# Performance work log

Hardware: AMD Instinct MI355X
Metric: run time of the kernel (lower is better)

The kernel has to match this reference:

```python
import jax, jax.numpy as jnp
import numpy as np

CLASSES = 100
SIGMA = 1.0
K_MIX = 11   # mixup pseudo-label kNN
K_KNN = 3    # knn regularizer


def _pairwise_sq(a, b):
    # ||a_i - b_j||^2 via Gram trick; a:[M,D], b:[N,D] -> [M,N]
    aa = jnp.sum(a * a, axis=1)[:, None]
    bb = jnp.sum(b * b, axis=1)[None, :]
    return aa + bb - 2.0 * (a @ b.T)


def _mode_rows(vals):
    # vals: [M,K] float labels. torch.mode semantics: most frequent value,
    # smallest value on ties.
    eq = vals[:, :, None] == vals[:, None, :]      # [M,K,K]
    counts = jnp.sum(eq.astype(vals.dtype), axis=2)  # [M,K]
    maxc = jnp.max(counts, axis=1, keepdims=True)
    masked = jnp.where(counts == maxc, vals, jnp.inf)
    return jnp.min(masked, axis=1)


def setup_inputs() -> dict:
    key = jax.random.key(0)
    k1, k2, k3, k4 = jax.random.split(key, 4)
    N, D = 4096, 512
    x = jax.random.normal(k1, (N, D), dtype=jnp.float32)
    y = jax.random.randint(k2, (N,), 0, CLASSES).astype(jnp.float32)
    lam = jax.random.beta(k3, 2.0, 2.0, (), dtype=jnp.float32)  # Beta(alpha=2, alpha=2)
    perm = jax.random.permutation(k4, N).astype(jnp.int32)
    return {"x": x, "y": y, "lam": lam, "perm": perm}


def reference(x, y, lam, perm):
    # ---- mixup branch: pseudo-label mixed samples via k=11 NN mode ----
    x_ul = x * lam + x[perm] * (1.0 - lam)              # [N,D]
    d = _pairwise_sq(x_ul, x)                            # [N,N]
    _, idx = jax.lax.top_k(-d, K_MIX)                    # indices of k smallest dists
    y_ul = _mode_rows(y[idx])                            # [N]
    x = jnp.concatenate([x, x_ul], axis=0)               # [2N,D]
    y = jnp.concatenate([y, y_ul], axis=0)               # [2N]

    num = x.shape[0]
    y_int = y.astype(jnp.int32)
    # per-class means (empty classes masked out, as the torch loop skips them)
    counts = jax.ops.segment_sum(jnp.ones((num,), x.dtype), y_int, num_segments=CLASSES)
    mu = jax.ops.segment_sum(x, y_int, num_segments=CLASSES) / jnp.maximum(counts, 1.0)[:, None]
    d2 = _pairwise_sq(x, mu)                             # [num, classes]
    pi = jnp.exp(-d2 / (2.0 * SIGMA ** 2)) * (counts > 0).astype(x.dtype)[None, :]
    yh = jax.nn.one_hot(y_int, CLASSES, dtype=x.dtype)
    eps = 1e-15
    pi = pi / (jnp.sum(pi, axis=1, keepdims=True) + eps)
    pi = jnp.clip(pi, 0.0, 1.0)
    loss_gm = jnp.mean(jnp.sum((pi - yh) ** 2, axis=1))

    # ---- knn regularizer: k=3 NN (excluding self) mode label, MSE ----
    dk = _pairwise_sq(x, x)                              # [num,num]
    _, idxk = jax.lax.top_k(-dk, K_KNN + 1)              # nearest is self (dist 0)
    y_ng = _mode_rows(y[idxk[:, 1:]])
    loss_knn = jnp.mean((y_ng - y) ** 2)
    return loss_gm + 0.01 * loss_knn
```

## Files before the change

### kernel.cpp

```cpp
#include <hip/hip_runtime.h>
#include <math.h>

#define N0   4096
#define D    512
#define NUM  8192
#define NCLS 100
#define KMIX 11

#define OFF_NALL   0
#define OFF_YALL   8192
#define OFF_RLOSS  16384
#define OFF_KSQ    24576
#define OFF_MUSUM  32768
#define OFF_CNT    83968
#define OFF_KNN    84096
#define ZERO_N     51344
#define OFF_NMU    84112
#define OFF_MUT    84224
#define OFF_TK1S   135424
#define OFF_TK1I   659712
#define OFF_TK2S   1184000
#define OFF_TK2I   1446144
#define OFF_XH     1708288
#define TOTAL_F    3805440
#define NEED_BYTES ((size_t)TOTAL_F * 4)

typedef _Float16 half8 __attribute__((ext_vector_type(8)));
typedef _Float16 half4v __attribute__((ext_vector_type(4)));
typedef float f32x4 __attribute__((ext_vector_type(4)));
typedef unsigned long long u64;

__device__ __forceinline__ float4 ld_row4(const float* __restrict__ x, const int* __restrict__ perm,
                                          float lam, float om, int r, int col) {
  if (r < N0) {
    return *(const float4*)(x + (size_t)r * D + col);
  } else {
    int rr = r - N0;
    int p = perm[rr];
    float4 a = *(const float4*)(x + (size_t)rr * D + col);
    float4 b = *(const float4*)(x + (size_t)p * D + col);
    float4 m;
    m.x = lam * a.x + om * b.x;  m.y = lam * a.y + om * b.y;
    m.z = lam * a.z + om * b.z;  m.w = lam * a.w + om * b.w;
    return m;
  }
}

__device__ __forceinline__ void gld_lds16(const _Float16* g, _Float16* l) {
  __builtin_amdgcn_global_load_lds(
      (const __attribute__((address_space(1))) void*)g,
      (__attribute__((address_space(3))) void*)l, 16, 0, 0);
}

__device__ __forceinline__ unsigned sortable(float s) {
  unsigned u = __float_as_uint(s);
  return ((int)u < 0) ? ~u : (u | 0x80000000u);
}
__device__ __forceinline__ float unsortable(unsigned u) {
  return __uint_as_float(((int)u < 0) ? (u & 0x7fffffffu) : ~u);
}

__global__ __launch_bounds__(256) void k_zero(float* __restrict__ p, int n) {
  int i = blockIdx.x * 256 + threadIdx.x;
  if (i < n) p[i] = 0.f;
}

__global__ __launch_bounds__(256) void k_y(const float* __restrict__ y, float* __restrict__ y_all) {
  int i = blockIdx.x * 256 + threadIdx.x;
  if (i < N0) y_all[i] = y[i];
}

__global__ __launch_bounds__(64) void k_prep(const float* __restrict__ x, const float* __restrict__ y,
                                             const int* __restrict__ perm, const float* __restrict__ lam_p,
                                             _Float16* __restrict__ Xh, float* __restrict__ n_all,
                                             float* __restrict__ y_all, float* __restrict__ accp,
                                             int* __restrict__ donep) {
  int i = blockIdx.x;
  float lam = lam_p[0], om = 1.0f - lam;
  int t = threadIdx.x;
  float4 a = ld_row4(x, perm, lam, om, i, t * 4);
  float4 b = ld_row4(x, perm, lam, om, i, t * 4 + 256);
  half4v ha, hb;
  ha.x = (_Float16)a.x; ha.y = (_Float16)a.y; ha.z = (_Float16)a.z; ha.w = (_Float16)a.w;
  hb.x = (_Float16)b.x; hb.y = (_Float16)b.y; hb.z = (_Float16)b.z; hb.w = (_Float16)b.w;
  *(half4v*)(Xh + (size_t)i * D + t * 4) = ha;
  *(half4v*)(Xh + (size_t)i * D + t * 4 + 256) = hb;
  float s = a.x*a.x + a.y*a.y + a.z*a.z + a.w*a.w
          + b.x*b.x + b.y*b.y + b.z*b.z + b.w*b.w;
  #pragma unroll
  for (int o = 32; o > 0; o >>= 1) s += __shfl_down(s, o, 64);
  if (t == 0) {
    n_all[i] = s;
    if (i < N0) y_all[i] = y[i];
    if (i == 0) { accp[0] = 0.f; donep[0] = 0; }
  }
}

template<int M, int NSPL>
__device__ __forceinline__ void knn_body(const _Float16* __restrict__ Xq,
                                         const _Float16* __restrict__ Xc,
                                         const float* __restrict__ nC,
                                         int cb0, int nctiles, int row0, int split,
                                         float* __restrict__ outS, int* __restrict__ outI,
                                         char* smem) {
  _Float16* Sh = (_Float16*)smem;
  u64* Lb = (u64*)smem;

  int tid = threadIdx.x;
  int wave = tid >> 6, lane = tid & 63;
  int wq = wave >> 1, wc = wave & 1;
  int col16 = lane & 15, quad = lane >> 4;

  const _Float16* q0 = Xq + (size_t)(wq * 32 + col16) * D + quad * 8;
  const _Float16* q1 = q0 + (size_t)16 * D;
  half8 aR[8][2][2];
  #pragma unroll
  for (int kt = 0; kt < 8; kt++)
    #pragma unroll
    for (int h = 0; h < 2; h++) {
      aR[kt][0][h] = *(const half8*)(q0 + kt * 64 + h * 32);
      aR[kt][1][h] = *(const half8*)(q1 + kt * 64 + h * 32);
    }

  u64 keys[M];
  #pragma unroll
  for (int q = 0; q < M; q++) keys[q] = ~0ULL;

  int r_scan = tid & 63, h_scan = tid >> 6;

  for (int ct = 0; ct < nctiles; ct++) {
    int c0 = cb0 + ct * 128;
    const _Float16* bb = Xc + (size_t)(c0 + wc * 64 + col16) * D + quad * 8;

    f32x4 acc[2][4];
    #pragma unroll
    for (int i = 0; i < 2; i++)
      #pragma unroll
      for (int j = 0; j < 4; j++) acc[i][j] = (f32x4){0.f, 0.f, 0.f, 0.f};

    #pragma unroll
    for (int kt = 0; kt < 8; kt++) {
      half8 b[4][2];
      #pragma unroll
      for (int j = 0; j < 4; j++)
        #pragma unroll
        for (int h = 0; h < 2; h++)
          b[j][h] = *(const half8*)(bb + (size_t)(j * 16) * D + kt * 64 + h * 32);
      #pragma unroll
      for (int h = 0; h < 2; h++)
        #pragma unroll
        for (int i = 0; i < 2; i++)
          #pragma unroll
          for (int j = 0; j < 4; j++)
            acc[i][j] = __builtin_amdgcn_mfma_f32_16x16x32_f16(aR[kt][i][h], b[j][h], acc[i][j], 0, 0, 0);
    }

    #pragma unroll
    for (int j = 0; j < 4; j++) {
      int cl = wc * 64 + j * 16 + col16;
      float ncv = nC[c0 + cl];
      #pragma unroll
      for (int i = 0; i < 2; i++) {
        half4v st;
        st.x = (_Float16)(ncv - 2.f * acc[i][j][0]);
        st.y = (_Float16)(ncv - 2.f * acc[i][j][1]);
        st.z = (_Float16)(ncv - 2.f * acc[i][j][2]);
        st.w = (_Float16)(ncv - 2.f * acc[i][j][3]);
        *(half4v*)&Sh[(size_t)cl * 68 + wq * 32 + i * 16 + quad * 4] = st;
      }
    }
    __syncthreads();

    for (int c = h_scan * 32; c < h_scan * 32 + 32; c++) {
      float s = (float)Sh[c * 68 + r_scan];
      u64 key = ((u64)sortable(s) << 32) | (unsigned)(c0 + c);
      if (key < keys[M - 1]) {
        keys[M - 1] = key;
        #pragma unroll
        for (int p = M - 1; p > 0; p--) {
          if (keys[p] < keys[p - 1]) { u64 tmp = keys[p]; keys[p] = keys[p - 1]; keys[p - 1] = tmp; }
        }
      }
    }
    __syncthreads();
  }

  #pragma unroll
  for (int q = 0; q < M; q++)
    Lb[((size_t)h_scan * 64 + r_scan) * M + q] = keys[q];
  __syncthreads();
  if (tid < 64) {
    int p0 = 0, p1 = 0, p2 = 0, p3 = 0;
    const u64* L0 = Lb + (size_t)(0 * 64 + tid) * M;
    const u64* L1 = Lb + (size_t)(1 * 64 + tid) * M;
    const u64* L2 = Lb + (size_t)(2 * 64 + tid) * M;
    const u64* L3 = Lb + (size_t)(3 * 64 + tid) * M;
    size_t off = (size_t)(row0 + tid) * ((size_t)NSPL * M) + (size_t)split * M;
    #pragma unroll
    for (int q = 0; q < M; q++) {
      u64 k0 = (p0 < M) ? L0[p0] : ~0ULL;
      u64 k1 = (p1 < M) ? L1[p1] : ~0ULL;
      u64 k2 = (p2 < M) ? L2[p2] : ~0ULL;
      u64 k3 = (p3 < M) ? L3[p3] : ~0ULL;
      u64 b01 = k0 < k1 ? k0 : k1;
      u64 b23 = k2 < k3 ? k2 : k3;
      u64 b = b01 < b23 ? b01 : b23;
      if (b == k0) p0++; else if (b == k1) p1++; else if (b == k2) p2++; else p3++;
      outS[off + q] = unsortable((unsigned)(b >> 32));
      outI[off + q] = (int)(unsigned)b;
    }
  }
}

__global__ __launch_bounds__(256, 2) void k_knn_all(const _Float16* __restrict__ Xh,
                                                    const float* __restrict__ n_all,
                                                    float* __restrict__ tk1s, int* __restrict__ tk1i,
                                                    float* __restrict__ tk2s, int* __restrict__ tk2i) {
  __shared__ __align__(16) char smem[32768];
  int bx = blockIdx.x;
  if (bx < 512) {
    int qblk = bx & 127, split = bx >> 7;
    knn_body<8, 4>(Xh + (size_t)(qblk * 64) * D, Xh, n_all,
                   split * 2048, 16, qblk * 64, split, tk2s, tk2i, smem);
  } else {
    int b = bx - 512;
    int qblk = b & 63, split = b >> 6;
    knn_body<16, 8>(Xh + (size_t)(N0 + qblk * 64) * D, Xh, n_all,
                    split * 512, 4, qblk * 64, split, tk1s, tk1i, smem);
  }
}

__global__ __launch_bounds__(256) void k_rr1(const float* __restrict__ x, const int* __restrict__ perm,
                                             const float* __restrict__ lam_p,
                                             const float* __restrict__ tks, const int* __restrict__ tki,
                                             const float* __restrict__ n_all, const float* __restrict__ y,
                                             float* __restrict__ y_all) {
  __shared__ u64 kl[128];
  __shared__ int sidx[16];
  __shared__ float sdot[16];
  int i = blockIdx.x;
  int t = threadIdx.x;
  float lam = lam_p[0], om = 1.f - lam;
  if (t < 128) {
    float s = tks[(size_t)i * 128 + t];
    int id = tki[(size_t)i * 128 + t];
    kl[t] = ((u64)sortable(s) << 32) | (unsigned)id;
  }
  __syncthreads();
  if (t < 128) {
    u64 me = kl[t];
    int rank = 0;
    for (int j = 0; j < 128; j++) rank += (kl[j] < me) ? 1 : 0;
    if (rank < 16) sidx[rank] = (int)(unsigned)me;
  }
  __syncthreads();
  int g = t >> 4, l16 = t & 15;
  int c = sidx[g];
  float dot = 0.f;
  for (int d0 = l16 * 4; d0 < D; d0 += 64) {
    float4 q4 = ld_row4(x, perm, lam, om, N0 + i, d0);
    float4 c4 = *(const float4*)(x + (size_t)c * D + d0);
    dot += q4.x*c4.x + q4.y*c4.y + q4.z*c4.z + q4.w*c4.w;
  }
  #pragma unroll
  for (int o = 8; o > 0; o >>= 1) dot += __shfl_down(dot, o, 16);
  if (l16 == 0) sdot[g] = n_all[c] - 2.f * dot;
  __syncthreads();
  if (t == 0) {
    float es[16]; int ei[16];
    for (int q = 0; q < 16; q++) { es[q] = sdot[q]; ei[q] = sidx[q]; }
    for (int a = 1; a < 16; a++) {
      float s = es[a]; int id = ei[a];
      int b = a - 1;
      while (b >= 0 && (es[b] > s || (es[b] == s && ei[b] > id))) {
        es[b + 1] = es[b]; ei[b + 1] = ei[b]; b--;
      }
      es[b + 1] = s; ei[b + 1] = id;
    }
    float lab[KMIX];
    for (int q = 0; q < KMIX; q++) lab[q] = y[ei[q]];
    float best = 3.0e38f; int bestc = 0;
    for (int q = 0; q < KMIX; q++) {
      int cnt = 0;
      for (int r = 0; r < KMIX; r++) cnt += (lab[r] == lab[q]) ? 1 : 0;
      if (cnt > bestc || (cnt == bestc && lab[q] < best)) { bestc = cnt; best = lab[q]; }
    }
    y_all[N0 + i] = best;
  }
}

__global__ __launch_bounds__(256) void k_post2(const float* __restrict__ x, const int* __restrict__ perm,
                                               const float* __restrict__ lam_p,
                                               const float* __restrict__ tks, const int* __restrict__ tki,
                                               const float* __restrict__ n_all, const float* __restrict__ y_all,
                                               float* __restrict__ ksq,
                                               _Float16* __restrict__ muH, float* __restrict__ nmu_pad,
                                               float* __restrict__ counts) {
  __shared__ __align__(16) char sm[33824];
  int bx = blockIdx.x;
  int t = threadIdx.x;
  float lam = lam_p[0], om = 1.f - lam;

  if (bx < NUM) {
    u64* kl = (u64*)sm;
    int* sidx = (int*)(sm + 256);
    float* sdot = (float*)(sm + 288);
    int i = bx;
    if (t < 32) {
      float s = tks[(size_t)i * 32 + t];
      int id = tki[(size_t)i * 32 + t];
      kl[t] = ((u64)sortable(s) << 32) | (unsigned)id;
    }
    __syncthreads();
    if (t < 32) {
      u64 me = kl[t];
      int rank = 0;
      #pragma unroll
      for (int j = 0; j < 32; j++) rank += (kl[j] < me) ? 1 : 0;
      if (rank < 8) sidx[rank] = (int)(unsigned)me;
    }
    __syncthreads();
    int g = t >> 5, l32 = t & 31;
    int c = sidx[g];
    float dot = 0.f;
    for (int d0 = l32 * 4; d0 < D; d0 += 128) {
      float4 q4 = ld_row4(x, perm, lam, om, i, d0);
      float4 c4 = ld_row4(x, perm, lam, om, c, d0);
      dot += q4.x*c4.x + q4.y*c4.y + q4.z*c4.z + q4.w*c4.w;
    }
    #pragma unroll
    for (int o = 16; o > 0; o >>= 1) dot += __shfl_down(dot, o, 32);
    if (l32 == 0) sdot[g] = n_all[c] - 2.f * dot;
    __syncthreads();
    if (t == 0) {
      float es[8]; int ei[8];
      for (int q = 0; q < 8; q++) { es[q] = sdot[q]; ei[q] = sidx[q]; }
      for (int a = 1; a < 8; a++) {
        float s = es[a]; int id = ei[a];
        int b = a - 1;
        while (b >= 0 && (es[b] > s || (es[b] == s && ei[b] > id))) {
          es[b + 1] = es[b]; ei[b + 1] = ei[b]; b--;
        }
        es[b + 1] = s; ei[b + 1] = id;
      }
      float l1 = y_all[ei[1]], l2 = y_all[ei[2]], l3 = y_all[ei[3]];
      int c1 = 1 + (int)(l2 == l1) + (int)(l3 == l1);
      int c2 = 1 + (int)(l1 == l2) + (int)(l3 == l2);
      int c3 = 1 + (int)(l1 == l3) + (int)(l2 == l3);
      int mc = c1 > c2 ? c1 : c2; mc = mc > c3 ? mc : c3;
      float mv = 3.0e38f;
      if (c1 == mc) mv = fminf(mv, l1);
      if (c2 == mc) mv = fminf(mv, l2);
      if (c3 == mc) mv = fminf(mv, l3);
      float d = mv - y_all[i];
      ksq[i] = d * d;
    }
  } else {
    int c = bx - NUM;
    int* lst = (int*)sm;
    float* red = (float*)(sm + 32768);
    int* cntp = (int*)(sm + 33792);
    if (c >= NCLS) {
      for (int d = t; d < D; d += 256) muH[(size_t)c * D + d] = (_Float16)0.f;
      if (t == 0) { nmu_pad[c] = 0.f; counts[c] = 0.f; }
      return;
    }
    float fc = (float)c;
    if (t == 0) cntp[0] = 0;
    __syncthreads();
    for (int i = t; i < NUM; i += 256) {
      if (y_all[i] == fc) {
        int pos = atomicAdd(cntp, 1);
        int p = (i >= N0) ? perm[i - N0] : 0;
        lst[pos] = i | (p << 13);
      }
    }
    __syncthreads();
    int n = cntp[0];
    float a0 = 0.f, a1 = 0.f;
    for (int m = 0; m < n; m++) {
      int v = lst[m];
      int i = v & 8191;
      if (i < N0) {
        a0 += x[(size_t)i * D + t];
        a1 += x[(size_t)i * D + t + 256];
      } else {
        int rr = i - N0, p = v >> 13;
        a0 += lam * x[(size_t)rr * D + t] + om * x[(size_t)p * D + t];
        a1 += lam * x[(size_t)rr * D + t + 256] + om * x[(size_t)p * D + t + 256];
      }
    }
    float inv = 1.f / fmaxf((float)n, 1.f);
    float v0 = a0 * inv, v1 = a1 * inv;
    muH[(size_t)c * D + t] = (_Float16)v0;
    muH[(size_t)c * D + t + 256] = (_Float16)v1;
    red[t] = v0 * v0 + v1 * v1;
    __syncthreads();
    for (int o = 128; o > 0; o >>= 1) { if (t < o) red[t] += red[t + o]; __syncthreads(); }
    if (t == 0) { nmu_pad[c] = red[0]; counts[c] = (float)n; }
  }
}

__global__ __launch_bounds__(256) void k_gm2f(const _Float16* __restrict__ Xh,
                                              const _Float16* __restrict__ muH,
                                              const float* __restrict__ nmu_pad,
                                              const float* __restrict__ counts,
                                              const float* __restrict__ n_all,
                                              const float* __restrict__ y_all,
                                              const float* __restrict__ ksq,
                                              float* __restrict__ accp, int* __restrict__ donep,
                                              float* __restrict__ out) {
  __shared__ __align__(16) char smem[49152];
  float* Ss = (float*)smem;
  _Float16* St = (_Float16*)smem;

  int tid = threadIdx.x;
  int wave = tid >> 6, lane = tid & 63;
  int wq = wave >> 1, wc = wave & 1;
  int col16 = lane & 15, quad = lane >> 4;
  int qb = blockIdx.x * 64;

  const _Float16* qg = Xh + (size_t)(qb + wave * 16 + col16) * D + quad * 8;
  int csegA = 2 * wave, csegB = 2 * wave + 1;
  const _Float16* cgA = muH + (size_t)(csegA * 16 + col16) * D + quad * 8;
  const _Float16* cgB = cgA + (size_t)16 * D;
  int ldsQ = wave * 1024 + lane * 8;
  int ldsCA = 4096 + csegA * 1024 + lane * 8;
  int ldsCB = 4096 + csegB * 1024 + lane * 8;

  f32x4 acc[2][4];
  #pragma unroll
  for (int i = 0; i < 2; i++)
    #pragma unroll
    for (int j = 0; j < 4; j++) acc[i][j] = (f32x4){0.f, 0.f, 0.f, 0.f};

  gld_lds16(qg,       St + ldsQ);
  gld_lds16(qg + 32,  St + ldsQ + 512);
  gld_lds16(cgA,      St + ldsCA);
  gld_lds16(cgA + 32, St + ldsCA + 512);
  gld_lds16(cgB,      St + ldsCB);
  gld_lds16(cgB + 32, St + ldsCB + 512);
  __syncthreads();

  #pragma unroll
  for (int t = 0; t < 8; t++) {
    const int cur = t & 1;
    if (t < 7) {
      int kk = (t + 1) * 64;
      _Float16* B = St + (cur ^ 1) * 12288;
      gld_lds16(qg + kk,       B + ldsQ);
      gld_lds16(qg + kk + 32,  B + ldsQ + 512);
      gld_lds16(cgA + kk,      B + ldsCA);
      gld_lds16(cgA + kk + 32, B + ldsCA + 512);
      gld_lds16(cgB + kk,      B + ldsCB);
      gld_lds16(cgB + kk + 32, B + ldsCB + 512);
    }
    const _Float16* Bc = St + cur * 12288;
    half8 a[2][2], b[4][2];
    #pragma unroll
    for (int i = 0; i < 2; i++)
      #pragma unroll
      for (int h = 0; h < 2; h++)
        a[i][h] = *(const half8*)(Bc + (wq * 2 + i) * 1024 + h * 512 + lane * 8);
    #pragma unroll
    for (int j = 0; j < 4; j++)
      #pragma unroll
      for (int h = 0; h < 2; h++)
        b[j][h] = *(const half8*)(Bc + 4096 + (wc * 4 + j) * 1024 + h * 512 + lane * 8);
    #pragma unroll
    for (int h = 0; h < 2; h++)
      #pragma unroll
      for (int i = 0; i < 2; i++)
        #pragma unroll
        for (int j = 0; j < 4; j++)
          acc[i][j] = __builtin_amdgcn_mfma_f32_16x16x32_f16(a[i][h], b[j][h], acc[i][j], 0, 0, 0);
    __syncthreads();
  }

  #pragma unroll
  for (int j = 0; j < 4; j++) {
    int c_local = wc * 64 + j * 16 + col16;
    float ncv = nmu_pad[c_local];
    #pragma unroll
    for (int i = 0; i < 2; i++) {
      float4 st;
      st.x = ncv - 2.f * acc[i][j][0];
      st.y = ncv - 2.f * acc[i][j][1];
      st.z = ncv - 2.f * acc[i][j][2];
      st.w = ncv - 2.f * acc[i][j][3];
      *(float4*)&Ss[(size_t)c_local * 68 + wq * 32 + i * 16 + quad * 4] = st;
    }
  }
  __syncthreads();

  int r = tid & 63, h = tid >> 6;
  float* redm = (float*)(smem + 35840);
  float* mrow = (float*)(smem + 36864);
  float* Sp   = (float*)(smem + 37120);
  float* Ep   = (float*)(smem + 38144);
  float* Yp   = (float*)(smem + 39168);
  float* Rf   = (float*)(smem + 40192);

  float mymin = 3.0e38f;
  for (int c = h * 32; c < h * 32 + 32; c++) {
    if (c < NCLS && counts[c] > 0.f) mymin = fminf(mymin, Ss[c * 68 + r]);
  }
  redm[h * 64 + r] = mymin;
  __syncthreads();
  if (tid < 64) {
    float ms = fminf(fminf(redm[tid], redm[64 + tid]), fminf(redm[128 + tid], redm[192 + tid]));
    mrow[tid] = ms;
  }
  __syncthreads();
  float ms = mrow[r];
  int yc = (int)y_all[qb + r];
  float Sv = 0.f, Se2 = 0.f, ey = 0.f;
  for (int c = h * 32; c < h * 32 + 32; c++) {
    if (c < NCLS && counts[c] > 0.f) {
      float e = expf(-0.5f * (Ss[c * 68 + r] - ms));
      Sv += e; Se2 += e * e;
      if (c == yc) ey = e;
    }
  }
  Sp[h * 64 + r] = Sv; Ep[h * 64 + r] = Se2; Yp[h * 64 + r] = ey;
  __syncthreads();
  if (tid < 64) {
    float S4 = Sp[tid] + Sp[64 + tid] + Sp[128 + tid] + Sp[192 + tid];
    float E4 = Ep[tid] + Ep[64 + tid] + Ep[128 + tid] + Ep[192 + tid];
    float Y4 = Yp[tid] + Yp[64 + tid] + Yp[128 + tid] + Yp[192 + tid];
    float m = n_all[qb + tid] + mrow[tid];
    float E = expf(-0.5f * m);
    float denom = E * S4 + 1e-15f;
    float f = E / denom;
    float row = E4 * f * f - 2.f * Y4 * f + 1.f + 0.01f * ksq[qb + tid];
    #pragma unroll
    for (int o = 32; o > 0; o >>= 1) row += __shfl_down(row, o, 64);
    Rf[tid] = row;
  }
  __syncthreads();
  if (tid == 0) {
    atomicAdd(accp, Rf[0]);
    __threadfence();
    int old = atomicAdd(donep, 1);
    if (old == (int)gridDim.x - 1) {
      float v = atomicAdd(accp, 0.0f);
      out[0] = v / (float)NUM;
    }
  }
}

#define QT 32
#define CTF 128
#define BKF 32

__global__ __launch_bounds__(64) void k_norms(const float* __restrict__ x, const int* __restrict__ perm,
                                              const float* __restrict__ lam_p, float* __restrict__ n_all) {
  int i = blockIdx.x;
  float lam = lam_p[0], om = 1.0f - lam;
  int t = threadIdx.x;
  float4 a = ld_row4(x, perm, lam, om, i, t * 4);
  float4 b = ld_row4(x, perm, lam, om, i, t * 4 + 256);
  float s = a.x*a.x + a.y*a.y + a.z*a.z + a.w*a.w
          + b.x*b.x + b.y*b.y + b.z*b.z + b.w*b.w;
  #pragma unroll
  for (int o = 32; o > 0; o >>= 1) s += __shfl_down(s, o, 64);
  if (t == 0) n_all[i] = s;
}

template<int KK>
__global__ __launch_bounds__(256) void k_knn_f32(const float* __restrict__ x, const int* __restrict__ perm,
                                                 const float* __restrict__ lam_p, int qstart,
                                                 const float* __restrict__ nC, int candPerSplit, int nsplits,
                                                 float* __restrict__ outS, int* __restrict__ outI) {
  __shared__ float Qs[BKF][QT + 4];
  __shared__ float Cs[BKF][CTF + 4];
  __shared__ float Sf[QT][CTF + 4];

  int tid = threadIdx.x;
  float lam = lam_p[0], om = 1.0f - lam;
  int qbase = blockIdx.x * QT;
  int cb = blockIdx.y * candPerSplit;
  int ce = cb + candPerSplit;

  int cx = tid & 31;
  int ry = tid >> 5;
  int lr = tid >> 3;
  int kc = (tid & 7) * 4;

  float ks[KK]; int ki[KK];
  #pragma unroll
  for (int q = 0; q < KK; q++) { ks[q] = 3.0e38f; ki[q] = 0x7fffffff; }

  for (int c0 = cb; c0 < ce; c0 += CTF) {
    float acc[4][4];
    #pragma unroll
    for (int i = 0; i < 4; i++)
      #pragma unroll
      for (int j = 0; j < 4; j++) acc[i][j] = 0.f;

    for (int kk = 0; kk < D; kk += BKF) {
      __syncthreads();
      {
        float4 v = ld_row4(x, perm, lam, om, qstart + qbase + lr, kk + kc);
        Qs[kc + 0][lr] = v.x; Qs[kc + 1][lr] = v.y; Qs[kc + 2][lr] = v.z; Qs[kc + 3][lr] = v.w;
      }
      #pragma unroll
      for (int rr = 0; rr < 4; rr++) {
        int r = lr + rr * 32;
        float4 v = ld_row4(x, perm, lam, om, c0 + r, kk + kc);
        Cs[kc + 0][r] = v.x; Cs[kc + 1][r] = v.y; Cs[kc + 2][r] = v.z; Cs[kc + 3][r] = v.w;
      }
      __syncthreads();
      #pragma unroll
      for (int k = 0; k < BKF; k++) {
        float4 a4 = *(const float4*)&Qs[k][ry * 4];
        float4 b4 = *(const float4*)&Cs[k][cx * 4];
        float av[4] = {a4.x, a4.y, a4.z, a4.w};
        float bv[4] = {b4.x, b4.y, b4.z, b4.w};
        #pragma unroll
        for (int i = 0; i < 4; i++)
          #pragma unroll
          for (int j = 0; j < 4; j++) acc[i][j] += av[i] * bv[j];
      }
    }
    __syncthreads();
    {
      float4 nc4 = *(const float4*)&nC[c0 + cx * 4];
      float ncv[4] = {nc4.x, nc4.y, nc4.z, nc4.w};
      #pragma unroll
      for (int i = 0; i < 4; i++)
        #pragma unroll
        for (int j = 0; j < 4; j++)
          Sf[ry * 4 + i][cx * 4 + j] = ncv[j] - 2.0f * acc[i][j];
    }
    __syncthreads();
    if (tid < QT) {
      for (int c = 0; c < CTF; c++) {
        float s = Sf[tid][c];
        int j = c0 + c;
        bool worse = (s > ks[KK - 1]) || (s == ks[KK - 1] && j > ki[KK - 1]);
        if (!worse) {
          ks[KK - 1] = s; ki[KK - 1] = j;
          #pragma unroll
          for (int p = KK - 1; p > 0; p--) {
            bool sw = (ks[p] < ks[p - 1]) || (ks[p] == ks[p - 1] && ki[p] < ki[p - 1]);
            if (sw) {
              float ts = ks[p]; ks[p] = ks[p - 1]; ks[p - 1] = ts;
              int ti = ki[p]; ki[p] = ki[p - 1]; ki[p - 1] = ti;
            }
          }
        }
      }
    }
  }

  if (tid < QT) {
    int row = qbase + tid;
    size_t off = (size_t)row * (nsplits * KK) + (size_t)blockIdx.y * KK;
    #pragma unroll
    for (int q = 0; q < KK; q++) { outS[off + q] = ks[q]; outI[off + q] = ki[q]; }
  }
}

__global__ __launch_bounds__(256) void k_final1(const float* __restrict__ tks, const int* __restrict__ tki,
                                                const float* __restrict__ y, float* __restrict__ y_all) {
  int i = blockIdx.x * 256 + threadIdx.x;
  if (i >= N0) return;
  const float* sb = tks + (size_t)i * 44;
  const int* ib = tki + (size_t)i * 44;
  int p0 = 0, p1 = 0, p2 = 0, p3 = 0;
  float lab[KMIX];
  #pragma unroll
  for (int q = 0; q < KMIX; q++) {
    float bs = 3.0e38f; int bi = 0x7fffffff; int w = 0;
    if (p0 < 11) { float s = sb[p0];      int id = ib[p0];      if (s < bs || (s == bs && id < bi)) { bs = s; bi = id; w = 0; } }
    if (p1 < 11) { float s = sb[11 + p1]; int id = ib[11 + p1]; if (s < bs || (s == bs && id < bi)) { bs = s; bi = id; w = 1; } }
    if (p2 < 11) { float s = sb[22 + p2]; int id = ib[22 + p2]; if (s < bs || (s == bs && id < bi)) { bs = s; bi = id; w = 2; } }
    if (p3 < 11) { float s = sb[33 + p3]; int id = ib[33 + p3]; if (s < bs || (s == bs && id < bi)) { bs = s; bi = id; w = 3; } }
    if (w == 0) p0++; else if (w == 1) p1++; else if (w == 2) p2++; else p3++;
    lab[q] = y[bi];
  }
  float best = 3.0e38f; int bestc = 0;
  #pragma unroll
  for (int q = 0; q < KMIX; q++) {
    int c = 0;
    #pragma unroll
    for (int r = 0; r < KMIX; r++) c += (lab[r] == lab[q]) ? 1 : 0;
    if (c > bestc || (c == bestc && lab[q] < best)) { bestc = c; best = lab[q]; }
  }
  y_all[N0 + i] = best;
}

__global__ __launch_bounds__(128) void k_stats(const float* __restrict__ x, const int* __restrict__ perm,
                                               const float* __restrict__ lam_p, const float* __restrict__ y_all,
                                               float* __restrict__ mu_sum, float* __restrict__ counts) {
  int i = blockIdx.x;
  float lam = lam_p[0], om = 1.0f - lam;
  int c = (int)y_all[i];
  float* ms = mu_sum + (size_t)c * D;
  int t = threadIdx.x;
  float4 v = ld_row4(x, perm, lam, om, i, t * 4);
  atomicAdd(&ms[t * 4 + 0], v.x);
  atomicAdd(&ms[t * 4 + 1], v.y);
  atomicAdd(&ms[t * 4 + 2], v.z);
  atomicAdd(&ms[t * 4 + 3], v.w);
  if (t == 0) atomicAdd(&counts[c], 1.0f);
}

__global__ __launch_bounds__(256) void k_mufin(const float* __restrict__ mu_sum, const float* __restrict__ counts,
                                               float* __restrict__ muT, float* __restrict__ nmu) {
  __shared__ float red[256];
  int c = blockIdx.x;
  float inv = 1.0f / fmaxf(counts[c], 1.0f);
  int t = threadIdx.x;
  float v0 = mu_sum[(size_t)c * D + t] * inv;
  float v1 = mu_sum[(size_t)c * D + t + 256] * inv;
  muT[(size_t)t * NCLS + c] = v0;
  muT[(size_t)(t + 256) * NCLS + c] = v1;
  red[t] = v0 * v0 + v1 * v1;
  __syncthreads();
  for (int o = 128; o > 0; o >>= 1) { if (t < o) red[t] += red[t + o]; __syncthreads(); }
  if (t == 0) nmu[c] = red[0];
}

__global__ __launch_bounds__(256) void k_final2(const float* __restrict__ t2s, const int* __restrict__ t2i,
                                                const float* __restrict__ y_all, float* __restrict__ knn_acc) {
  __shared__ float red[256];
  int i = blockIdx.x * 256 + threadIdx.x;
  float dd2 = 0.f;
  if (i < NUM) {
    const float* sA = t2s + (size_t)i * 8; const float* sB = sA + 4;
    const int* iA = t2i + (size_t)i * 8;   const int* iB = iA + 4;
    int pa = 0, pb = 0;
    int midx[4];
    #pragma unroll
    for (int q = 0; q < 4; q++) {
      float sa = (pa < 4) ? sA[pa] : 3.0e38f;
      float sb = (pb < 4) ? sB[pb] : 3.0e38f;
      int ia = (pa < 4) ? iA[pa] : 0x7fffffff;
      int ib = (pb < 4) ? iB[pb] : 0x7fffffff;
      bool ta = (sa < sb) || (sa == sb && ia < ib);
      midx[q] = ta ? ia : ib;
      if (ta) pa++; else pb++;
    }
    float l1 = y_all[midx[1]], l2 = y_all[midx[2]], l3 = y_all[midx[3]];
    int c1 = 1 + (int)(l2 == l1) + (int)(l3 == l1);
    int c2 = 1 + (int)(l1 == l2) + (int)(l3 == l2);
    int c3 = 1 + (int)(l1 == l3) + (int)(l2 == l3);
    int mc = c1 > c2 ? c1 : c2; mc = mc > c3 ? mc : c3;
    float mv = 3.0e38f;
    if (c1 == mc) mv = fminf(mv, l1);
    if (c2 == mc) mv = fminf(mv, l2);
    if (c3 == mc) mv = fminf(mv, l3);
    float d = mv - y_all[i];
    dd2 = d * d;
  }
  red[threadIdx.x] = dd2;
  __syncthreads();
  for (int o = 128; o > 0; o >>= 1) { if (threadIdx.x < o) red[threadIdx.x] += red[threadIdx.x + o]; __syncthreads(); }
  if (threadIdx.x == 0) atomicAdd(knn_acc, red[0]);
}

__global__ __launch_bounds__(128) void k_gm(const float* __restrict__ x, const int* __restrict__ perm,
                                            const float* __restrict__ lam_p, const float* __restrict__ y_all,
                                            const float* __restrict__ n_all, const float* __restrict__ muT,
                                            const float* __restrict__ nmu, const float* __restrict__ counts,
                                            float* __restrict__ row_loss) {
  __shared__ float red[128];
  int i = blockIdx.x;
  int t = threadIdx.x;
  float lam = lam_p[0], om = 1.0f - lam;
  bool valid = (t < NCLS) && (counts[t] > 0.f);
  float d2 = 3.0e38f;
  if (t < NCLS) {
    float dot = 0.f;
    for (int d = 0; d < D; d += 4) {
      float4 v = ld_row4(x, perm, lam, om, i, d);
      dot += v.x * muT[(size_t)(d + 0) * NCLS + t];
      dot += v.y * muT[(size_t)(d + 1) * NCLS + t];
      dot += v.z * muT[(size_t)(d + 2) * NCLS + t];
      dot += v.w * muT[(size_t)(d + 3) * NCLS + t];
    }
    d2 = n_all[i] + nmu[t] - 2.f * dot;
  }
  red[t] = valid ? d2 : 3.0e38f;
  __syncthreads();
  for (int o = 64; o > 0; o >>= 1) { if (t < o) red[t] = fminf(red[t], red[t + o]); __syncthreads(); }
  float m = red[0];
  __syncthreads();
  float e = valid ? expf(-0.5f * (d2 - m)) : 0.f;
  red[t] = e;
  __syncthreads();
  for (int o = 64; o > 0; o >>= 1) { if (t < o) red[t] += red[t + o]; __syncthreads(); }
  float S = red[0];
  __syncthreads();
  float E = expf(-0.5f * m);
  float denom = E * S + 1e-15f;
  float pi = e * E / denom;
  pi = fminf(fmaxf(pi, 0.f), 1.f);
  int yc = (int)y_all[i];
  float term = pi * pi - 2.f * ((t == yc) ? pi : 0.f);
  red[t] = valid ? term : 0.f;
  __syncthreads();
  for (int o = 64; o > 0; o >>= 1) { if (t < o) red[t] += red[t + o]; __syncthreads(); }
  if (t == 0) row_loss[i] = red[0] + 1.0f;
}

__global__ __launch_bounds__(256) void k_final_slow(const float* __restrict__ row_loss,
                                                    const float* __restrict__ knn_acc, float* __restrict__ out) {
  __shared__ float red[256];
  int t = threadIdx.x;
  float s = 0.f;
  for (int i = t; i < NUM; i += 256) s += row_loss[i];
  red[t] = s;
  __syncthreads();
  for (int o = 128; o > 0; o >>= 1) { if (t < o) red[t] += red[t + o]; __syncthreads(); }
  if (t == 0) out[0] = red[0] / (float)NUM + 0.01f * (knn_acc[0] / (float)NUM);
}

extern "C" void kernel_launch(void* const* d_in, const int* in_sizes, int n_in,
                              void* d_out, int out_size, void* d_ws, size_t ws_size,
                              hipStream_t stream) {
  const float* x   = (const float*)d_in[0];
  const float* y   = (const float*)d_in[1];
  const float* lam = (const float*)d_in[2];
  const int* perm  = (const int*)d_in[3];
  float* ws = (float*)d_ws;

  float* n_all  = ws + OFF_NALL;
  float* y_all  = ws + OFF_YALL;
  float* rloss  = ws + OFF_RLOSS;
  float* ksq    = ws + OFF_KSQ;
  float* mu_sum = ws + OFF_MUSUM;
  float* counts = ws + OFF_CNT;
  float* knn_acc= ws + OFF_KNN;
  float* nmu    = ws + OFF_NMU;
  float* muT    = ws + OFF_MUT;
  float* tk1s   = ws + OFF_TK1S;
  int*   tk1i   = (int*)(ws + OFF_TK1I);
  float* tk2s   = ws + OFF_TK2S;
  int*   tk2i   = (int*)(ws + OFF_TK2I);
  _Float16* Xh  = (_Float16*)(ws + OFF_XH);
  _Float16* muH = (_Float16*)(ws + OFF_MUSUM);
  float* nmu_pad= ws + OFF_MUT;
  float* accp   = ws + OFF_KNN;
  int*   donep  = (int*)(ws + OFF_KNN + 1);

  bool fast = ws_size >= NEED_BYTES;

  if (fast) {
    k_prep<<<NUM, 64, 0, stream>>>(x, y, perm, lam, Xh, n_all, y_all, accp, donep);
    k_knn_all<<<1024, 256, 0, stream>>>(Xh, n_all, tk1s, tk1i, tk2s, tk2i);
    k_rr1<<<N0, 256, 0, stream>>>(x, perm, lam, tk1s, tk1i, n_all, y, y_all);
    k_post2<<<NUM + 128, 256, 0, stream>>>(x, perm, lam, tk2s, tk2i, n_all, y_all,
                                           ksq, muH, nmu_pad, counts);
    k_gm2f<<<NUM / 64, 256, 0, stream>>>(Xh, muH, nmu_pad, counts, n_all, y_all,
                                         ksq, accp, donep, (float*)d_out);
  } else {
    k_y<<<(N0 + 255) / 256, 256, 0, stream>>>(y, y_all);
    k_zero<<<(ZERO_N + 255) / 256, 256, 0, stream>>>(mu_sum, ZERO_N);
    k_norms<<<NUM, 64, 0, stream>>>(x, perm, lam, n_all);
    dim3 g1(N0 / QT, 4);
    k_knn_f32<KMIX><<<g1, 256, 0, stream>>>(x, perm, lam, N0, n_all, N0 / 4, 4, tk1s, tk1i);
    k_final1<<<(N0 + 255) / 256, 256, 0, stream>>>(tk1s, tk1i, y, y_all);
    k_stats<<<NUM, 128, 0, stream>>>(x, perm, lam, y_all, mu_sum, counts);
    k_mufin<<<NCLS, 256, 0, stream>>>(mu_sum, counts, muT, nmu);
    dim3 g2(NUM / QT, 2);
    k_knn_f32<4><<<g2, 256, 0, stream>>>(x, perm, lam, 0, n_all, NUM / 2, 2, tk2s, tk2i);
    k_final2<<<NUM / 256, 256, 0, stream>>>(tk2s, tk2i, y_all, knn_acc);
    k_gm<<<NUM, 128, 0, stream>>>(x, perm, lam, y_all, n_all, muT, nmu, counts, rloss);
    k_final_slow<<<1, 256, 0, stream>>>(rloss, knn_acc, (float*)d_out);
  }
}
```

Measured before the change: 783.3 us.

## Fuse mixup and self kNN candidate scans with LDS double-buffered MFMA tiles

The two separate kNN passes over the 8192-row concatenated set are merged. Mixed-sample query rows now compute one distance tile against 1024-column splits of all candidates and feed both the top-8 list (self kNN) and a top-16 list (mixup kNN restricted to splits covering the original rows), so the mixup distances are no longer recomputed. Query and candidate fragments are streamed through double-buffered LDS with direct global-to-LDS loads instead of being held in registers, and occupancy is raised to 3 blocks per CU. This adds extra sort work in the scan loop and a per-k-step barrier, and changes the candidate counts the rerank kernels merge.

Result: faster. 689.2 us (-12.0%).

```diff
diff --git a/kernel.cpp b/kernel.cpp
--- a/kernel.cpp
+++ b/kernel.cpp
@@ -18,9 +18,9 @@
 #define OFF_NMU    84112
 #define OFF_MUT    84224
 #define OFF_TK1S   135424
-#define OFF_TK1I   659712
-#define OFF_TK2S   1184000
-#define OFF_TK2I   1446144
+#define OFF_TK1I   397568
+#define OFF_TK2S   659712
+#define OFF_TK2I   1184000
 #define OFF_XH     1708288
 #define TOTAL_F    3805440
 #define NEED_BYTES ((size_t)TOTAL_F * 4)
@@ -96,14 +96,15 @@
   }
 }
 
-template<int M, int NSPL>
-__device__ __forceinline__ void knn_body(const _Float16* __restrict__ Xq,
-                                         const _Float16* __restrict__ Xc,
-                                         const float* __restrict__ nC,
-                                         int cb0, int nctiles, int row0, int split,
-                                         float* __restrict__ outS, int* __restrict__ outI,
-                                         char* smem) {
-  _Float16* Sh = (_Float16*)smem;
+__device__ __forceinline__ void knn_body_fused(
+    const _Float16* __restrict__ Xq, const _Float16* __restrict__ Xc,
+    const float* __restrict__ nC, int cb0, int nctiles,
+    int row0, int split, bool mix, int mixrow0,
+    float* __restrict__ outS, int* __restrict__ outI,
+    float* __restrict__ outS2, int* __restrict__ outI2,
+    char* smem) {
+  _Float16* St = (_Float16*)smem;
+  _Float16* Sh = (_Float16*)(smem + 24576);
   u64* Lb = (u64*)smem;
 
   int tid = threadIdx.x;
@@ -111,26 +112,34 @@
   int wq = wave >> 1, wc = wave & 1;
   int col16 = lane & 15, quad = lane >> 4;
 
-  const _Float16* q0 = Xq + (size_t)(wq * 32 + col16) * D + quad * 8;
-  const _Float16* q1 = q0 + (size_t)16 * D;
-  half8 aR[8][2][2];
-  #pragma unroll
-  for (int kt = 0; kt < 8; kt++)
-    #pragma unroll
-    for (int h = 0; h < 2; h++) {
-      aR[kt][0][h] = *(const half8*)(q0 + kt * 64 + h * 32);
-      aR[kt][1][h] = *(const half8*)(q1 + kt * 64 + h * 32);
-    }
-
-  u64 keys[M];
-  #pragma unroll
-  for (int q = 0; q < M; q++) keys[q] = ~0ULL;
+  const _Float16* qg = Xq + (size_t)(wave * 16 + col16) * D + quad * 8;
+  int csegA = 2 * wave, csegB = 2 * wave + 1;
+  int ldsQ = wave * 1024 + lane * 8;
+  int ldsCA = 4096 + csegA * 1024 + lane * 8;
+  int ldsCB = 4096 + csegB * 1024 + lane * 8;
+
+  u64 keys[8];
+  #pragma unroll
+  for (int q = 0; q < 8; q++) keys[q] = ~0ULL;
+  u64 keys2[16];
+  #pragma unroll
+  for (int q = 0; q < 16; q++) keys2[q] = ~0ULL;
 
   int r_scan = tid & 63, h_scan = tid >> 6;
+
+  {
+    const _Float16* cA = Xc + (size_t)(cb0 + csegA * 16 + col16) * D + quad * 8;
+    const _Float16* cB = cA + (size_t)16 * D;
+    gld_lds16(qg,      St + ldsQ);  gld_lds16(qg + 32, St + ldsQ + 512);
+    gld_lds16(cA,      St + ldsCA); gld_lds16(cA + 32, St + ldsCA + 512);
+    gld_lds16(cB,      St + ldsCB); gld_lds16(cB + 32, St + ldsCB + 512);
+  }
+  __syncthreads();
 
   for (int ct = 0; ct < nctiles; ct++) {
     int c0 = cb0 + ct * 128;
-    const _Float16* bb = Xc + (size_t)(c0 + wc * 64 + col16) * D + quad * 8;
+    const _Float16* cgA = Xc + (size_t)(c0 + csegA * 16 + col16) * D + quad * 8;
+    const _Float16* cgB = cgA + (size_t)16 * D;
 
     f32x4 acc[2][4];
     #pragma unroll
@@ -139,20 +148,41 @@
       for (int j = 0; j < 4; j++) acc[i][j] = (f32x4){0.f, 0.f, 0.f, 0.f};
 
     #pragma unroll
-    for (int kt = 0; kt < 8; kt++) {
-      half8 b[4][2];
+    for (int t = 0; t < 8; t++) {
+      const int cur = t & 1;
+      if (t < 7) {
+        int kk = (t + 1) * 64;
+        _Float16* B = St + (cur ^ 1) * 12288;
+        gld_lds16(qg + kk,       B + ldsQ);  gld_lds16(qg + kk + 32,  B + ldsQ + 512);
+        gld_lds16(cgA + kk,      B + ldsCA); gld_lds16(cgA + kk + 32, B + ldsCA + 512);
+        gld_lds16(cgB + kk,      B + ldsCB); gld_lds16(cgB + kk + 32, B + ldsCB + 512);
+      } else if (ct + 1 < nctiles) {
+        const _Float16* nA = cgA + (size_t)128 * D;
+        const _Float16* nB = cgB + (size_t)128 * D;
+        gld_lds16(qg,      St + ldsQ);  gld_lds16(qg + 32, St + ldsQ + 512);
+        gld_lds16(nA,      St + ldsCA); gld_lds16(nA + 32, St + ldsCA + 512);
+        gld_lds16(nB,      St + ldsCB); gld_lds16(nB + 32, St + ldsCB + 512);
+      }
+      const _Float16* Bc = St + cur * 12288;
+      half8 a[2][2], b[4][2];
+      #pragma unroll
+      for (int i = 0; i < 2; i++)
+        #pragma unroll
+        for (int h = 0; h < 2; h++)
+          a[i][h] = *(const half8*)(Bc + (wq * 2 + i) * 1024 + h * 512 + lane * 8);
       #pragma unroll
       for (int j = 0; j < 4; j++)
         #pragma unroll
         for (int h = 0; h < 2; h++)
-          b[j][h] = *(const half8*)(bb + (size_t)(j * 16) * D + kt * 64 + h * 32);
+          b[j][h] = *(const half8*)(Bc + 4096 + (wc * 4 + j) * 1024 + h * 512 + lane * 8);
       #pragma unroll
       for (int h = 0; h < 2; h++)
         #pragma unroll
         for (int i = 0; i < 2; i++)
           #pragma unroll
           for (int j = 0; j < 4; j++)
-            acc[i][j] = __builtin_amdgcn_mfma_f32_16x16x32_f16(aR[kt][i][h], b[j][h], acc[i][j], 0, 0, 0);
+            acc[i][j] = __builtin_amdgcn_mfma_f32_16x16x32_f16(a[i][h], b[j][h], acc[i][j], 0, 0, 0);
+      __syncthreads();
     }
 
     #pragma unroll
@@ -174,34 +204,41 @@
     for (int c = h_scan * 32; c < h_scan * 32 + 32; c++) {
       float s = (float)Sh[c * 68 + r_scan];
       u64 key = ((u64)sortable(s) << 32) | (unsigned)(c0 + c);
-      if (key < keys[M - 1]) {
-        keys[M - 1] = key;
+      if (key < keys[7]) {
+        keys[7] = key;
         #pragma unroll
-        for (int p = M - 1; p > 0; p--) {
+        for (int p = 7; p > 0; p--) {
           if (keys[p] < keys[p - 1]) { u64 tmp = keys[p]; keys[p] = keys[p - 1]; keys[p - 1] = tmp; }
         }
       }
-    }
-    __syncthreads();
-  }
-
-  #pragma unroll
-  for (int q = 0; q < M; q++)
-    Lb[((size_t)h_scan * 64 + r_scan) * M + q] = keys[q];
+      if (mix && key < keys2[15]) {
+        keys2[15] = key;
+        #pragma unroll
+        for (int p = 15; p > 0; p--) {
+          if (keys2[p] < keys2[p - 1]) { u64 tmp = keys2[p]; keys2[p] = keys2[p - 1]; keys2[p - 1] = tmp; }
+        }
+      }
+    }
+    __syncthreads();
+  }
+
+  #pragma unroll
+  for (int q = 0; q < 8; q++)
+    Lb[((size_t)h_scan * 64 + r_scan) * 8 + q] = keys[q];
   __syncthreads();
   if (tid < 64) {
     int p0 = 0, p1 = 0, p2 = 0, p3 = 0;
-    const u64* L0 = Lb + (size_t)(0 * 64 + tid) * M;
-    const u64* L1 = Lb + (size_t)(1 * 64 + tid) * M;
-    const u64* L2 = Lb + (size_t)(2 * 64 + tid) * M;
-    const u64* L3 = Lb + (size_t)(3 * 64 + tid) * M;
-    size_t off = (size_t)(row0 + tid) * ((size_t)NSPL * M) + (size_t)split * M;
-    #pragma unroll
-    for (int q = 0; q < M; q++) {
-      u64 k0 = (p0 < M) ? L0[p0] : ~0ULL;
-      u64 k1 = (p1 < M) ? L1[p1] : ~0ULL;
-      u64 k2 = (p2 < M) ? L2[p2] : ~0ULL;
-      u64 k3 = (p3 < M) ? L3[p3] : ~0ULL;
+    const u64* L0 = Lb + (size_t)(0 * 64 + tid) * 8;
+    const u64* L1 = Lb + (size_t)(1 * 64 + tid) * 8;
+    const u64* L2 = Lb + (size_t)(2 * 64 + tid) * 8;
+    const u64* L3 = Lb + (size_t)(3 * 64 + tid) * 8;
+    size_t off = (size_t)(row0 + tid) * 64 + (size_t)split * 8;
+    #pragma unroll
+    for (int q = 0; q < 8; q++) {
+      u64 k0 = (p0 < 8) ? L0[p0] : ~0ULL;
+      u64 k1 = (p1 < 8) ? L1[p1] : ~0ULL;
+      u64 k2 = (p2 < 8) ? L2[p2] : ~0ULL;
+      u64 k3 = (p3 < 8) ? L3[p3] : ~0ULL;
       u64 b01 = k0 < k1 ? k0 : k1;
       u64 b23 = k2 < k3 ? k2 : k3;
       u64 b = b01 < b23 ? b01 : b23;
@@ -210,24 +247,54 @@
       outI[off + q] = (int)(unsigned)b;
     }
   }
-}
-
-__global__ __launch_bounds__(256, 2) void k_knn_all(const _Float16* __restrict__ Xh,
+
+  if (mix) {
+    __syncthreads();
+    #pragma unroll
+    for (int q = 0; q < 16; q++)
+      Lb[((size_t)h_scan * 64 + r_scan) * 16 + q] = keys2[q];
+    __syncthreads();
+    if (tid < 64) {
+      int p0 = 0, p1 = 0, p2 = 0, p3 = 0;
+      const u64* L0 = Lb + (size_t)(0 * 64 + tid) * 16;
+      const u64* L1 = Lb + (size_t)(1 * 64 + tid) * 16;
+      const u64* L2 = Lb + (size_t)(2 * 64 + tid) * 16;
+      const u64* L3 = Lb + (size_t)(3 * 64 + tid) * 16;
+      size_t off = (size_t)(mixrow0 + tid) * 64 + (size_t)split * 16;
+      #pragma unroll
+      for (int q = 0; q < 16; q++) {
+        u64 k0 = (p0 < 16) ? L0[p0] : ~0ULL;
+        u64 k1 = (p1 < 16) ? L1[p1] : ~0ULL;
+        u64 k2 = (p2 < 16) ? L2[p2] : ~0ULL;
+        u64 k3 = (p3 < 16) ? L3[p3] : ~0ULL;
+        u64 b01 = k0 < k1 ? k0 : k1;
+        u64 b23 = k2 < k3 ? k2 : k3;
+        u64 b = b01 < b23 ? b01 : b23;
+        if (b == k0) p0++; else if (b == k1) p1++; else if (b == k2) p2++; else p3++;
+        outS2[off + q] = unsortable((unsigned)(b >> 32));
+        outI2[off + q] = (int)(unsigned)b;
+      }
+    }
+  }
+}
+
+__global__ __launch_bounds__(256, 3) void k_knn_all(const _Float16* __restrict__ Xh,
                                                     const float* __restrict__ n_all,
                                                     float* __restrict__ tk1s, int* __restrict__ tk1i,
                                                     float* __restrict__ tk2s, int* __restrict__ tk2i) {
-  __shared__ __align__(16) char smem[32768];
+  __shared__ __align__(16) char smem[49152];
   int bx = blockIdx.x;
-  if (bx < 512) {
-    int qblk = bx & 127, split = bx >> 7;
-    knn_body<8, 4>(Xh + (size_t)(qblk * 64) * D, Xh, n_all,
-                   split * 2048, 16, qblk * 64, split, tk2s, tk2i, smem);
+  int qblk, split; bool mix;
+  if (bx < 256) {
+    qblk = 64 + (bx & 63); split = bx >> 6; mix = true;
   } else {
-    int b = bx - 512;
-    int qblk = b & 63, split = b >> 6;
-    knn_body<16, 8>(Xh + (size_t)(N0 + qblk * 64) * D, Xh, n_all,
-                    split * 512, 4, qblk * 64, split, tk1s, tk1i, smem);
-  }
+    int r = bx - 256;
+    if (r < 256) { qblk = r & 63; split = r >> 6; mix = false; }
+    else { int r2 = r - 256; split = 4 + (r2 >> 7); qblk = r2 & 127; mix = false; }
+  }
+  knn_body_fused(Xh + (size_t)(qblk * 64) * D, Xh, n_all,
+                 split * 1024, 8, qblk * 64, split, mix, (qblk - 64) * 64,
+                 tk2s, tk2i, tk1s, tk1i, smem);
 }
 
 __global__ __launch_bounds__(256) void k_rr1(const float* __restrict__ x, const int* __restrict__ perm,
@@ -235,22 +302,23 @@
                                              const float* __restrict__ tks, const int* __restrict__ tki,
                                              const float* __restrict__ n_all, const float* __restrict__ y,
                                              float* __restrict__ y_all) {
-  __shared__ u64 kl[128];
+  __shared__ u64 kl[64];
   __shared__ int sidx[16];
   __shared__ float sdot[16];
   int i = blockIdx.x;
   int t = threadIdx.x;
   float lam = lam_p[0], om = 1.f - lam;
-  if (t < 128) {
-    float s = tks[(size_t)i * 128 + t];
-    int id = tki[(size_t)i * 128 + t];
+  if (t < 64) {
+    float s = tks[(size_t)i * 64 + t];
+    int id = tki[(size_t)i * 64 + t];
     kl[t] = ((u64)sortable(s) << 32) | (unsigned)id;
   }
   __syncthreads();
-  if (t < 128) {
+  if (t < 64) {
     u64 me = kl[t];
     int rank = 0;
-    for (int j = 0; j < 128; j++) rank += (kl[j] < me) ? 1 : 0;
+    #pragma unroll
+    for (int j = 0; j < 64; j++) rank += (kl[j] < me) ? 1 : 0;
     if (rank < 16) sidx[rank] = (int)(unsigned)me;
   }
   __syncthreads();
@@ -303,20 +371,20 @@
 
   if (bx < NUM) {
     u64* kl = (u64*)sm;
-    int* sidx = (int*)(sm + 256);
-    float* sdot = (float*)(sm + 288);
+    int* sidx = (int*)(sm + 512);
+    float* sdot = (float*)(sm + 544);
     int i = bx;
-    if (t < 32) {
-      float s = tks[(size_t)i * 32 + t];
-      int id = tki[(size_t)i * 32 + t];
+    if (t < 64) {
+      float s = tks[(size_t)i * 64 + t];
+      int id = tki[(size_t)i * 64 + t];
       kl[t] = ((u64)sortable(s) << 32) | (unsigned)id;
     }
     __syncthreads();
-    if (t < 32) {
+    if (t < 64) {
       u64 me = kl[t];
       int rank = 0;
       #pragma unroll
-      for (int j = 0; j < 32; j++) rank += (kl[j] < me) ? 1 : 0;
+      for (int j = 0; j < 64; j++) rank += (kl[j] < me) ? 1 : 0;
       if (rank < 8) sidx[rank] = (int)(unsigned)me;
     }
     __syncthreads();
```
